# Kernel optimization log

Hardware: AMD Instinct MI355X
Metric: run time of the kernel (lower is better)

## Reference

```python
import jax, jax.numpy as jnp
import numpy as np

N, E = 25000, 400000
IN, HID, OUT = 128, 256, 128
T = 4                      # towers
F1, F2 = HID // T, OUT // T  # per-tower out dims (divide_input=False)
A = 12                     # len(aggregators)=4 * len(scalers)=3
EPS_STD = 1e-5
EPS_BN = 1e-5


def _glorot(k, shape):
    fin, fout = shape[-2], shape[-1]
    lim = float(np.sqrt(6.0 / (fin + fout)))
    return jax.random.uniform(k, shape, jnp.float32, -lim, lim)


def setup_inputs():
    key = jax.random.key(0)
    ks = jax.random.split(key, 10)
    x = jax.random.normal(ks[0], (N, IN), jnp.float32)
    edge_index = jax.random.randint(ks[1], (2, E), 0, N, dtype=jnp.int32)
    # avg_deg['log'] buffer of PNAConv: mean over nodes of log(deg+1)
    deg = jax.ops.segment_sum(jnp.ones((E,), jnp.float32), edge_index[1], num_segments=N)
    avg_log = jnp.mean(jnp.log(deg + 1.0)).astype(jnp.float32)
    return dict(
        x=x, edge_index=edge_index, avg_log=avg_log,
        pre1_W=_glorot(ks[2], (T, 2 * IN, F1)), pre1_b=jnp.zeros((T, F1), jnp.float32),
        post1_W=_glorot(ks[3], (T, IN + A * F1, F1)), post1_b=jnp.zeros((T, F1), jnp.float32),
        lin1_W=_glorot(ks[4], (T * F1, HID)), lin1_b=jnp.zeros((HID,), jnp.float32),
        bn1_g=jnp.ones((HID,), jnp.float32), bn1_b=jnp.zeros((HID,), jnp.float32),
        pre2_W=_glorot(ks[5], (T, 2 * HID, F2)), pre2_b=jnp.zeros((T, F2), jnp.float32),
        post2_W=_glorot(ks[6], (T, HID + A * F2, F2)), post2_b=jnp.zeros((T, F2), jnp.float32),
        lin2_W=_glorot(ks[7], (T * F2, OUT)), lin2_b=jnp.zeros((OUT,), jnp.float32),
        bn2_g=jnp.ones((OUT,), jnp.float32), bn2_b=jnp.zeros((OUT,), jnp.float32),
    )


def _pna(x, src, tgt, preW, preB, postW, postB, linW, linB, avg_log):
    """PNAConv: towers=T, divide_input=False, pre_layers=post_layers=1,
    aggregators [mean,min,max,std], scalers [identity,amplification,attenuation]."""
    n = x.shape[0]
    # message: per tower Linear on concat([x_i, x_j]) where i=target, j=source
    h = jnp.concatenate([x[tgt], x[src]], axis=-1)            # [E, 2*F_in]
    msg = jnp.einsum('ec,tcf->etf', h, preW) + preB           # [E, T, F]
    ones = jnp.ones((msg.shape[0],), msg.dtype)
    deg = jax.ops.segment_sum(ones, tgt, num_segments=n)      # in-degree [n]
    degc = jnp.maximum(deg, 1.0)[:, None, None]
    s1 = jax.ops.segment_sum(msg, tgt, num_segments=n)
    mean = s1 / degc
    s2 = jax.ops.segment_sum(msg * msg, tgt, num_segments=n)
    var = jnp.maximum(s2 / degc - mean * mean, 0.0)
    std = jnp.sqrt(var + EPS_STD)
    has = (deg > 0.0)[:, None, None]
    mn = jnp.where(has, jax.ops.segment_min(msg, tgt, num_segments=n), 0.0)
    mx = jnp.where(has, jax.ops.segment_max(msg, tgt, num_segments=n), 0.0)
    agg = jnp.concatenate([mean, mn, mx, std], axis=-1)       # [n, T, 4F]
    dlog = jnp.log(jnp.maximum(deg, 1.0) + 1.0)[:, None, None]
    out = jnp.concatenate([agg, agg * (dlog / avg_log), agg * (avg_log / dlog)], axis=-1)  # [n, T, 12F]
    xt = jnp.broadcast_to(x[:, None, :], (n, T, x.shape[-1]))
    post_in = jnp.concatenate([xt, out], axis=-1)             # [n, T, F_in + 12F]
    post = jnp.einsum('ntc,tcf->ntf', post_in, postW) + postB # [n, T, F]
    return post.reshape(n, -1) @ linW + linB                  # [n, out]


def _bn(x, g, b):
    # BatchNorm1d training-mode math: biased batch variance
    m = jnp.mean(x, axis=0)
    v = jnp.mean((x - m) ** 2, axis=0)
    return g * (x - m) / jnp.sqrt(v + EPS_BN) + b


def reference(x, edge_index, avg_log, pre1_W, pre1_b, post1_W, post1_b, lin1_W, lin1_b,
              bn1_g, bn1_b, pre2_W, pre2_b, post2_W, post2_b, lin2_W, lin2_b, bn2_g, bn2_b):
    src, tgt = edge_index[0], edge_index[1]
    h = _pna(x, src, tgt, pre1_W, pre1_b, post1_W, post1_b, lin1_W, lin1_b, avg_log)
    h = jax.nn.relu(_bn(jnp.nan_to_num(h), bn1_g, bn1_b))
    h = _pna(h, src, tgt, pre2_W, pre2_b, post2_W, post2_b, lin2_W, lin2_b, avg_log)
    h = jax.nn.relu(_bn(jnp.nan_to_num(h), bn2_g, bn2_b))
    return h
```

## Files before the change

### kernel.cpp

```cpp
#include <hip/hip_runtime.h>
#include <hip/hip_bf16.h>
#include <float.h>
#include <math.h>

typedef __hip_bfloat16 bf16;
typedef __attribute__((ext_vector_type(8))) short short8;
typedef __attribute__((ext_vector_type(4))) float f32x4;

__device__ __forceinline__ float bf2f(bf16 v){ return __bfloat162float(v); }
__device__ __forceinline__ void stv(float* p, float v){ *p = v; }
__device__ __forceinline__ void stv(bf16* p, float v){ *p = __float2bfloat16(v); }
__device__ __forceinline__ float nanfix(float v){
  if (v != v) return 0.f;
  return fminf(fmaxf(v, -FLT_MAX), FLT_MAX);
}
__device__ __forceinline__ unsigned short f2bu(float f){
  unsigned u = __float_as_uint(f);
  unsigned r = u + 0x7FFFu + ((u>>16)&1u);
  return (unsigned short)(r>>16);
}
template<int VEC>
__device__ __forceinline__ void ldbf(const bf16* p, float (&o)[VEC]){
  if constexpr (VEC==4){
    ushort4 r = *(const ushort4*)p;
    o[0]=__uint_as_float((unsigned)r.x<<16); o[1]=__uint_as_float((unsigned)r.y<<16);
    o[2]=__uint_as_float((unsigned)r.z<<16); o[3]=__uint_as_float((unsigned)r.w<<16);
  } else {
    ushort2 r = *(const ushort2*)p;
    o[0]=__uint_as_float((unsigned)r.x<<16); o[1]=__uint_as_float((unsigned)r.y<<16);
  }
}

__global__ void k_scan1(const int* __restrict__ deg, int* __restrict__ bsum, int N){
  __shared__ int sm[256];
  int i = blockIdx.x*256 + threadIdx.x;
  sm[threadIdx.x] = (i < N) ? deg[i] : 0;
  __syncthreads();
  for (int off = 128; off > 0; off >>= 1){
    if (threadIdx.x < off) sm[threadIdx.x] += sm[threadIdx.x + off];
    __syncthreads();
  }
  if (threadIdx.x == 0) bsum[blockIdx.x] = sm[0];
}

__global__ void k_scan2(int* __restrict__ bsum, int NB){
  __shared__ int sm[1024];
  int tid = threadIdx.x;
  sm[tid] = (tid < NB) ? bsum[tid] : 0;
  __syncthreads();
  for (int off = 1; off < 1024; off <<= 1){
    int t = (tid >= off) ? sm[tid-off] : 0;
    __syncthreads();
    sm[tid] += t;
    __syncthreads();
  }
  if (tid < NB) bsum[tid] = (tid == 0) ? 0 : sm[tid-1];
}

__global__ void k_scan3(const int* __restrict__ deg, const int* __restrict__ bsum,
                        int* __restrict__ offs, int N){
  __shared__ int sm[256];
  int tid = threadIdx.x;
  int i = blockIdx.x*256 + tid;
  int v = (i < N) ? deg[i] : 0;
  sm[tid] = v; __syncthreads();
  for (int off = 1; off < 256; off <<= 1){
    int t = (tid >= off) ? sm[tid-off] : 0;
    __syncthreads();
    sm[tid] += t;
    __syncthreads();
  }
  if (i < N) offs[i+1] = bsum[blockIdx.x] + sm[tid];
  if (i == 0) offs[0] = 0;
}

__global__ void k_scatter(const int* __restrict__ src, const int* __restrict__ tgt,
                          const int* __restrict__ offs, int* __restrict__ cnt,
                          int* __restrict__ ssrc, int E){
  int e = blockIdx.x*blockDim.x + threadIdx.x;
  if (e < E){
    int t = tgt[e];
    int pos = offs[t] + atomicAdd(&cnt[t], 1);
    ssrc[pos] = src[e];
  }
}

__device__ __forceinline__ void rp_pqT(const float* preW, const float* preB,
                                       bf16* WpqT, float* bpq, int K, int F, int idx){
  int NC = 4*F;
  int total = 2*NC*K;
  if (idx < total){
    int j = idx/K, c = idx%K;
    int half = j/NC, jj = j%NC, t = jj/F, f = jj%F;
    WpqT[idx] = __float2bfloat16(preW[(t*2*K + half*K + c)*F + f]);
  }
  if (idx < 2*NC) bpq[idx] = (idx < NC) ? preB[idx] : 0.f;
}
__device__ __forceinline__ void rp_xT(const float* postW, const float* postB,
                                      bf16* WxT, float* bpost, int KX, int F, int idx){
  int NC = 4*F; int KP = KX + 12*F;
  if (idx < NC*KX){
    int j = idx/KX, c = idx%KX, t = j/F, f = j%F;
    WxT[idx] = __float2bfloat16(postW[(t*KP + c)*F + f]);
  }
  if (idx < NC) bpost[idx] = postB[idx];
}
__device__ __forceinline__ void rp_agg3(const float* postW, bf16* Wagg3,
                                        int KX, int F, int idx){
  int K4F = 4*F; int KP = KX + 12*F;
  int total = 4*3*F*K4F;
  if (idx < total){
    int k = idx % K4F; int r = idx / K4F;
    int zr = r % (3*F); int t = r / (3*F);
    int s = zr / F, f = zr % F;
    Wagg3[idx] = __float2bfloat16(postW[((size_t)(t*KP + KX + s*K4F + k))*F + f]);
  }
}
__device__ __forceinline__ void rp_linT(const float* linW, bf16* WlinT,
                                        int K, int NC, int idx){
  if (idx < NC*K){
    int j = idx/K, c = idx%K;
    WlinT[idx] = __float2bfloat16(linW[c*NC + j]);
  }
}

struct SetupArgs {
  const float *pre1W, *pre1b, *post1W, *post1b, *lin1W;
  const float *pre2W, *pre2b, *post2W, *post2b, *lin2W;
  const float *x;
  const int *tgt;
  bf16 *WpqT1, *WxT1, *Wagg31, *lin1WT;
  bf16 *WpqT2, *WxT2, *Wagg32, *lin2WT;
  bf16 *x_bf;
  int *deg;
  float *bpq1, *bpost1, *bpq2, *bpost2;
  int nx4;
  int E;
  int gstride;
};

__global__ void k_setup(SetupArgs a){
  int idx = blockIdx.x*256 + threadIdx.x;
  switch (blockIdx.y){
    case 0: rp_pqT (a.pre1W, a.pre1b, a.WpqT1, a.bpq1, 128, 64, idx); break;
    case 1: rp_xT  (a.post1W, a.post1b, a.WxT1, a.bpost1, 128, 64, idx); break;
    case 2: rp_agg3(a.post1W, a.Wagg31, 128, 64, idx); break;
    case 3: rp_linT(a.lin1W, a.lin1WT, 256, 256, idx); break;
    case 4: rp_pqT (a.pre2W, a.pre2b, a.WpqT2, a.bpq2, 256, 32, idx); break;
    case 5: rp_xT  (a.post2W, a.post2b, a.WxT2, a.bpost2, 256, 32, idx); break;
    case 6: rp_agg3(a.post2W, a.Wagg32, 256, 32, idx); break;
    case 7: rp_linT(a.lin2W, a.lin2WT, 128, 128, idx); break;
    case 8:
      for (int i = idx; i < a.nx4; i += a.gstride){
        float4 v = *(const float4*)(a.x + (size_t)i*4);
        ushort4 o = make_ushort4(f2bu(v.x), f2bu(v.y), f2bu(v.z), f2bu(v.w));
        *(ushort4*)(a.x_bf + (size_t)i*4) = o;
      }
      break;
    case 9:
      for (int e = idx; e < a.E; e += a.gstride)
        atomicAdd(&a.deg[a.tgt[e]], 1);
      break;
  }
}

template<typename TO, bool STATS>
__global__ __launch_bounds__(256) void k_mgemm(
    const bf16* __restrict__ A, int lda,
    const bf16* __restrict__ Bt,
    const float* __restrict__ bias,
    TO* __restrict__ Cout, int ldc,
    int N, int K, int NC, float* __restrict__ part)
{
  __shared__ __align__(16) bf16 As[64*40];
  __shared__ __align__(16) bf16 Bs[64*40];
  __shared__ float sstat[4][2][16][2];
  int n0 = blockIdx.y*64;
  int j0 = blockIdx.x*64;
  int tid = threadIdx.x;
  int srow = tid>>2, skoff = (tid&3)*8;
  int wave = tid>>6, lane = tid&63;
  int wy = (wave>>1)*32, wx = (wave&1)*32;
  int l15 = lane&15, q = lane>>4;
  f32x4 acc[2][2] = {};
  for (int k0 = 0; k0 < K; k0 += 32){
    uint4 av = {0,0,0,0};
    int ar = n0 + srow;
    if (ar < N) av = *(const uint4*)(A + (size_t)ar*lda + k0 + skoff);
    *(uint4*)&As[srow*40 + skoff] = av;
    uint4 bv = {0,0,0,0};
    int br = j0 + srow;
    if (br < NC) bv = *(const uint4*)(Bt + (size_t)br*K + k0 + skoff);
    *(uint4*)&Bs[srow*40 + skoff] = bv;
    __syncthreads();
    short8 af[2], bfr[2];
    #pragma unroll
    for (int i = 0; i < 2; i++){
      af[i]  = *(const short8*)&As[(wy + i*16 + l15)*40 + q*8];
      bfr[i] = *(const short8*)&Bs[(wx + i*16 + l15)*40 + q*8];
    }
    #pragma unroll
    for (int mi = 0; mi < 2; mi++)
      #pragma unroll
      for (int ni = 0; ni < 2; ni++)
        acc[mi][ni] = __builtin_amdgcn_mfma_f32_16x16x32_bf16(af[mi], bfr[ni], acc[mi][ni], 0, 0, 0);
    __syncthreads();
  }
  float cs[2] = {0.f, 0.f}, cq[2] = {0.f, 0.f};
  #pragma unroll
  for (int mi = 0; mi < 2; mi++){
    #pragma unroll
    for (int ni = 0; ni < 2; ni++){
      #pragma unroll
      for (int r = 0; r < 4; r++){
        int n  = n0 + wy + mi*16 + q*4 + r;
        int jj = j0 + wx + ni*16 + l15;
        if (n < N && jj < NC){
          float v = acc[mi][ni][r] + bias[jj];
          stv(&Cout[(size_t)n*ldc + jj], v);
          if constexpr (STATS){ cs[ni] += v; cq[ni] = fmaf(v, v, cq[ni]); }
        }
      }
    }
  }
  if constexpr (STATS){
    #pragma unroll
    for (int ni = 0; ni < 2; ni++){
      float s = cs[ni], qq = cq[ni];
      s  += __shfl_xor(s, 16);  s  += __shfl_xor(s, 32);
      qq += __shfl_xor(qq, 16); qq += __shfl_xor(qq, 32);
      if (q == 0){ sstat[wave][ni][l15][0] = s; sstat[wave][ni][l15][1] = qq; }
    }
    __syncthreads();
    if (tid < 64){
      int j = tid;
      int wa = (j < 32) ? 0 : 1, wb = wa + 2;
      int ni = (j & 31) >> 4, li = j & 15;
      float s  = sstat[wa][ni][li][0] + sstat[wb][ni][li][0];
      float qq = sstat[wa][ni][li][1] + sstat[wb][ni][li][1];
      part[(size_t)blockIdx.y*2*ldc + (j0 + j)]       = s;
      part[(size_t)blockIdx.y*2*ldc + ldc + (j0 + j)] = qq;
    }
  }
}

template<int COLS>
__global__ __launch_bounds__(256) void k_postagg(
    const bf16* __restrict__ agg,
    const bf16* __restrict__ Wagg3,
    const bf16* __restrict__ PQX, int ldq, int cinOff,
    const float* __restrict__ scal,
    bf16* __restrict__ Cout, int ldc, int N)
{
  constexpr int K4F = 4*COLS;
  constexpr int ROWS3 = 3*COLS;
  constexpr int NI = COLS/32;
  constexpr int LDA_AGG = 16*COLS;
  __shared__ __align__(16) bf16 As[64*40];
  __shared__ __align__(16) bf16 Bs[ROWS3*40];
  int z = blockIdx.z;
  int n0 = blockIdx.y*64;
  int tid = threadIdx.x;
  int srow = tid>>2, skoff = (tid&3)*8;
  int wave = tid>>6, lane = tid&63;
  int wy = (wave>>1)*32;
  int wx = (wave&1)*(COLS/2);
  int l15 = lane&15, q = lane>>4;
  f32x4 acc[2][NI][3] = {};
  const bf16* Az = agg + (size_t)z*K4F;
  const bf16* Bz = Wagg3 + (size_t)z*ROWS3*K4F;
  for (int k0 = 0; k0 < K4F; k0 += 32){
    uint4 av = {0,0,0,0};
    int ar = n0 + srow;
    if (ar < N) av = *(const uint4*)(Az + (size_t)ar*LDA_AGG + k0 + skoff);
    *(uint4*)&As[srow*40 + skoff] = av;
    for (int r = srow; r < ROWS3; r += 64){
      uint4 bv = *(const uint4*)(Bz + (size_t)r*K4F + k0 + skoff);
      *(uint4*)&Bs[r*40 + skoff] = bv;
    }
    __syncthreads();
    short8 af[2];
    #pragma unroll
    for (int i = 0; i < 2; i++)
      af[i] = *(const short8*)&As[(wy + i*16 + l15)*40 + q*8];
    #pragma unroll
    for (int s = 0; s < 3; s++){
      #pragma unroll
      for (int ni = 0; ni < NI; ni++){
        short8 bfr = *(const short8*)&Bs[(s*COLS + wx + ni*16 + l15)*40 + q*8];
        #pragma unroll
        for (int mi = 0; mi < 2; mi++)
          acc[mi][ni][s] = __builtin_amdgcn_mfma_f32_16x16x32_bf16(af[mi], bfr, acc[mi][ni][s], 0, 0, 0);
      }
    }
    __syncthreads();
  }
  #pragma unroll
  for (int mi = 0; mi < 2; mi++){
    #pragma unroll
    for (int ni = 0; ni < NI; ni++){
      int jj = wx + ni*16 + l15;
      int jg = z*COLS + jj;
      #pragma unroll
      for (int r = 0; r < 4; r++){
        int n = n0 + wy + mi*16 + q*4 + r;
        if (n < N){
          float s1 = scal[2*n], s2 = scal[2*n+1];
          float cin = bf2f(PQX[(size_t)n*ldq + cinOff + jg]);
          float v = cin + acc[mi][ni][0][r] + s1*acc[mi][ni][1][r] + s2*acc[mi][ni][2][r];
          Cout[(size_t)n*ldc + jg] = __float2bfloat16(v);
        }
      }
    }
  }
}

template<int NC, int F>
__global__ __launch_bounds__(256) void k_agg(const bf16* __restrict__ PQ, int lda,
    const int* __restrict__ ssrc, const int* __restrict__ offs,
    const float* __restrict__ avgp,
    bf16* __restrict__ agg, float* __restrict__ scal, int N){
  constexpr int VEC = NC/64;
  int wave = threadIdx.x>>6, lane = threadIdx.x&63;
  int n = blockIdx.x*4 + wave;
  if (n >= N) return;
  int c0 = lane*VEC;
  float p[VEC];
  ldbf<VEC>(PQ + (size_t)n*lda + c0, p);
  int s0 = offs[n], s1 = offs[n+1];
  float sum[VEC], sq[VEC], mn[VEC], mx[VEC];
  #pragma unroll
  for (int v=0;v<VEC;v++){ sum[v]=0.f; sq[v]=0.f; mn[v]=FLT_MAX; mx[v]=-FLT_MAX; }
  const bf16* Q = PQ + NC + c0;
  int i = s0;
  for (; i+7 < s1; i += 8){
    int se[8];
    #pragma unroll
    for (int u=0;u<8;u++) se[u] = ssrc[i+u];
    float qv[8][VEC];
    #pragma unroll
    for (int u=0;u<8;u++) ldbf<VEC>(Q + (size_t)se[u]*lda, qv[u]);
    #pragma unroll
    for (int u=0;u<8;u++){
      #pragma unroll
      for (int v=0;v<VEC;v++){
        float qq = qv[u][v];
        sum[v] += qq; sq[v] = fmaf(qq,qq,sq[v]);
        mn[v] = fminf(mn[v], qq); mx[v] = fmaxf(mx[v], qq);
      }
    }
  }
  for (; i+3 < s1; i += 4){
    int se[4];
    #pragma unroll
    for (int u=0;u<4;u++) se[u] = ssrc[i+u];
    float qv[4][VEC];
    #pragma unroll
    for (int u=0;u<4;u++) ldbf<VEC>(Q + (size_t)se[u]*lda, qv[u]);
    #pragma unroll
    for (int u=0;u<4;u++){
      #pragma unroll
      for (int v=0;v<VEC;v++){
        float qq = qv[u][v];
        sum[v] += qq; sq[v] = fmaf(qq,qq,sq[v]);
        mn[v] = fminf(mn[v], qq); mx[v] = fmaxf(mx[v], qq);
      }
    }
  }
  for (; i < s1; i++){
    int sa = ssrc[i];
    float qa[VEC];
    ldbf<VEC>(Q + (size_t)sa*lda, qa);
    #pragma unroll
    for (int v=0;v<VEC;v++){
      float qq = qa[v];
      sum[v]+=qq; sq[v]=fmaf(qq,qq,sq[v]); mn[v]=fminf(mn[v],qq); mx[v]=fmaxf(mx[v],qq);
    }
  }
  int deg = s1-s0;
  float degf = (float)deg;
  float degc = fmaxf(degf, 1.f);
  unsigned short um[VEC], un[VEC], ux[VEC], us[VEC];
  #pragma unroll
  for (int v=0;v<VEC;v++){
    float pv = p[v];
    float sum_m = fmaf(degf, pv, sum[v]);
    float sq_m  = sq[v] + 2.f*pv*sum[v] + degf*pv*pv;
    float mean = sum_m/degc;
    float var = fmaxf(sq_m/degc - mean*mean, 0.f);
    float sd = sqrtf(var + 1e-5f);
    float mnv = deg>0 ? pv + mn[v] : 0.f;
    float mxv = deg>0 ? pv + mx[v] : 0.f;
    um[v]=f2bu(mean); un[v]=f2bu(mnv); ux[v]=f2bu(mxv); us[v]=f2bu(sd);
  }
  int t = c0 / F, f0 = c0 % F;
  bf16* base = agg + (size_t)n*4*NC + (size_t)t*4*F + f0;
  if constexpr (VEC==4){
    *(ushort4*)(base)       = make_ushort4(um[0],um[1],um[2],um[3]);
    *(ushort4*)(base + F)   = make_ushort4(un[0],un[1],un[2],un[3]);
    *(ushort4*)(base + 2*F) = make_ushort4(ux[0],ux[1],ux[2],ux[3]);
    *(ushort4*)(base + 3*F) = make_ushort4(us[0],us[1],us[2],us[3]);
  } else {
    *(ushort2*)(base)       = make_ushort2(um[0],um[1]);
    *(ushort2*)(base + F)   = make_ushort2(un[0],un[1]);
    *(ushort2*)(base + 2*F) = make_ushort2(ux[0],ux[1]);
    *(ushort2*)(base + 3*F) = make_ushort2(us[0],us[1]);
  }
  if (lane==0){
    float dlog = logf(degc + 1.f);
    float avg = *avgp;
    scal[2*n]   = dlog/avg;
    scal[2*n+1] = avg/dlog;
  }
}

template<int C>
__global__ __launch_bounds__(256) void k_bn_final(const float* __restrict__ part, int PB,
                                                  float* __restrict__ stats){
  int c = blockIdx.x*256 + threadIdx.x;
  if (c >= 2*C) return;
  int CH = gridDim.y;
  int per = (PB + CH - 1)/CH;
  int p0 = blockIdx.y*per, p1 = min(p0 + per, PB);
  float acc = 0.f;
  int p = p0;
  for (; p+4 <= p1; p += 4){
    acc += part[(size_t)p*2*C + c] + part[(size_t)(p+1)*2*C + c]
         + part[(size_t)(p+2)*2*C + c] + part[(size_t)(p+3)*2*C + c];
  }
  for (; p < p1; p++) acc += part[(size_t)p*2*C + c];
  atomicAdd(&stats[c], acc);
}

template<typename TO, int C>
__global__ void k_bn_apply(const bf16* __restrict__ h, const float* __restrict__ stats,
     const float* __restrict__ g, const float* __restrict__ b,
     TO* __restrict__ out, int N){
  int idx = blockIdx.x*blockDim.x + threadIdx.x;
  if (idx >= N*(C/4)) return;
  int c = (idx % (C/4))*4;
  float fn = (float)N;
  float v[4];
  ldbf<4>(h + (size_t)idx*4, v);
  float r[4];
  #pragma unroll
  for (int k = 0; k < 4; k++){
    float m = stats[c+k]/fn;
    float var = fmaxf(stats[C+c+k]/fn - m*m, 0.f);
    float inv = rsqrtf(var + 1e-5f);
    float vv = nanfix(v[k]);
    r[k] = fmaxf(g[c+k]*(vv - m)*inv + b[c+k], 0.f);
  }
  if constexpr (sizeof(TO) == 4){
    float4 o = {r[0], r[1], r[2], r[3]};
    *(float4*)((float*)out + (size_t)idx*4) = o;
  } else {
    ushort4 o = make_ushort4(f2bu(r[0]), f2bu(r[1]), f2bu(r[2]), f2bu(r[3]));
    *(ushort4*)((bf16*)out + (size_t)idx*4) = o;
  }
}

static inline int cdiv(int a, int b){ return (a + b - 1)/b; }

extern "C" void kernel_launch(void* const* d_in, const int* in_sizes, int n_in,
                              void* d_out, int out_size, void* d_ws, size_t ws_size,
                              hipStream_t stream){
  const int IN = 128, HID = 256, T = 4, F1 = 64, F2 = 32;
  const int N = in_sizes[0]/IN;
  const int E = in_sizes[1]/2;
  const int NC1 = T*F1;
  const int NC2 = T*F2;
  const int LDQ1 = 2*NC1 + NC1;
  const int LDQ2 = 2*NC2 + NC2;

  const float* x      = (const float*)d_in[0];
  const int*   ei     = (const int*)  d_in[1];
  const int*   srcE   = ei;
  const int*   tgtE   = ei + E;
  const float* avgp   = (const float*)d_in[2];
  const float* pre1W  = (const float*)d_in[3];
  const float* pre1b  = (const float*)d_in[4];
  const float* post1W = (const float*)d_in[5];
  const float* post1b = (const float*)d_in[6];
  const float* lin1W  = (const float*)d_in[7];
  const float* lin1b  = (const float*)d_in[8];
  const float* bn1g   = (const float*)d_in[9];
  const float* bn1b   = (const float*)d_in[10];
  const float* pre2W  = (const float*)d_in[11];
  const float* pre2b  = (const float*)d_in[12];
  const float* post2W = (const float*)d_in[13];
  const float* post2b = (const float*)d_in[14];
  const float* lin2W  = (const float*)d_in[15];
  const float* lin2b  = (const float*)d_in[16];
  const float* bn2g   = (const float*)d_in[17];
  const float* bn2b   = (const float*)d_in[18];

  char* w = (char*)d_ws;
  auto alloc = [&](size_t bytes)->void*{
    void* p = (void*)w; w += (bytes + 255) & ~(size_t)255; return p;
  };
  bf16* BT1    = (bf16*)alloc((size_t)LDQ1*IN*2);
  bf16* WpqT1  = BT1;              bf16* WxT1 = BT1 + (size_t)2*NC1*IN;
  float* bias1 = (float*)alloc((size_t)LDQ1*4);
  float* bpq1  = bias1;            float* bpost1 = bias1 + 2*NC1;
  bf16* Wagg31 = (bf16*)alloc((size_t)T*3*F1*4*F1*2);
  bf16* lin1WT = (bf16*)alloc((size_t)HID*NC1*2);
  bf16* BT2    = (bf16*)alloc((size_t)LDQ2*HID*2);
  bf16* WpqT2  = BT2;              bf16* WxT2 = BT2 + (size_t)2*NC2*HID;
  float* bias2 = (float*)alloc((size_t)LDQ2*4);
  float* bpq2  = bias2;            float* bpost2 = bias2 + 2*NC2;
  bf16* Wagg32 = (bf16*)alloc((size_t)T*3*F2*4*F2*2);
  bf16* lin2WT = (bf16*)alloc((size_t)128*NC2*2);
  int* deg_i   = (int*)alloc((size_t)N*4);
  int* cnt     = (int*)alloc((size_t)N*4);
  float* stats = (float*)alloc(1024*4);
  size_t zbytes = (size_t)((char*)stats - (char*)deg_i) + 1024*4;
  int* offs    = (int*)alloc((size_t)(N+1)*4);
  int* bsum    = (int*)alloc((size_t)cdiv(N,256)*4);
  int* ssrc    = (int*)alloc((size_t)E*4);
  bf16* x_bf   = (bf16*)alloc((size_t)N*IN*2);
  bf16* PQX    = (bf16*)alloc((size_t)N*LDQ1*2);
  bf16* aggb   = (bf16*)alloc((size_t)N*4*NC1*2);
  float* scal  = (float*)alloc((size_t)N*2*4);
  bf16* postbb = (bf16*)alloc((size_t)N*256*2);
  bf16* hpre   = (bf16*)alloc((size_t)N*256*2);
  bf16* h1b    = (bf16*)alloc((size_t)N*256*2);
  int NB = cdiv(N,64);
  float* part  = (float*)alloc((size_t)NB*512*4);

  hipMemsetAsync(deg_i, 0, zbytes, stream);

  int sgx = cdiv(T*3*F1*4*F1, 256);
  SetupArgs sa = { pre1W, pre1b, post1W, post1b, lin1W,
                   pre2W, pre2b, post2W, post2b, lin2W,
                   x, tgtE,
                   WpqT1, WxT1, Wagg31, lin1WT,
                   WpqT2, WxT2, Wagg32, lin2WT,
                   x_bf, deg_i,
                   bpq1, bpost1, bpq2, bpost2,
                   N*IN/4, E, sgx*256 };
  k_setup<<<dim3(sgx, 10),256,0,stream>>>(sa);

  int NBs = cdiv(N,256);
  k_scan1<<<NBs,256,0,stream>>>(deg_i, bsum, N);
  k_scan2<<<1,1024,0,stream>>>(bsum, NBs);
  k_scan3<<<NBs,256,0,stream>>>(deg_i, bsum, offs, N);
  k_scatter<<<cdiv(E,256),256,0,stream>>>(srcE, tgtE, offs, cnt, ssrc, E);

  k_mgemm<bf16,false><<<dim3(LDQ1/64,NB),256,0,stream>>>(x_bf, IN, BT1, bias1, PQX, LDQ1, N, IN, LDQ1, nullptr);
  k_agg<256,64><<<cdiv(N,4),256,0,stream>>>(PQX, LDQ1, ssrc, offs, avgp, aggb, scal, N);
  k_postagg<64><<<dim3(1,NB,T),256,0,stream>>>(aggb, Wagg31, PQX, LDQ1, 2*NC1, scal,
                                               postbb, NC1, N);
  k_mgemm<bf16,true><<<dim3(4,NB),256,0,stream>>>(postbb, NC1, lin1WT, lin1b, hpre, HID, N, NC1, HID, part);
  k_bn_final<256><<<dim3(2,4),256,0,stream>>>(part, NB, stats);
  k_bn_apply<bf16,256><<<cdiv(N*64,256),256,0,stream>>>(hpre, stats, bn1g, bn1b, h1b, N);

  k_mgemm<bf16,false><<<dim3(LDQ2/64,NB),256,0,stream>>>(h1b, HID, BT2, bias2, PQX, LDQ2, N, HID, LDQ2, nullptr);
  k_agg<128,32><<<cdiv(N,4),256,0,stream>>>(PQX, LDQ2, ssrc, offs, avgp, aggb, scal, N);
  k_postagg<32><<<dim3(1,NB,T),256,0,stream>>>(aggb, Wagg32, PQX, LDQ2, 2*NC2, scal,
                                               postbb, NC2, N);
  k_mgemm<bf16,true><<<dim3(2,NB),256,0,stream>>>(postbb, NC2, lin2WT, lin2b, hpre, 128, N, NC2, 128, part);
  k_bn_final<128><<<dim3(1,4),256,0,stream>>>(part, NB, stats + 512);
  k_bn_apply<float,128><<<cdiv(N*32,256),256,0,stream>>>(hpre, stats + 512, bn2g, bn2b, (float*)d_out, N);
}
```

Baseline: 371.6 us.

## Double-buffer GEMM tiles with direct global-to-LDS async loads

Both the message/linear GEMM kernel and the post-aggregation GEMM kernel now load A and B tiles with global_load_lds straight into LDS instead of going through registers. The tiles are double-buffered so the next k-step's load is issued while the current step's MFMAs run, hiding global-memory latency. In exchange, the LDS row padding is removed (stride 32 instead of 40), which can add bank conflicts on fragment reads. The row-bounds checks on A and B are also gone, so the last partial row tile now reads past N unless the buffers are padded.

```diff
diff --git a/kernel.cpp b/kernel.cpp
--- a/kernel.cpp
+++ b/kernel.cpp
@@ -29,6 +29,12 @@
     ushort2 r = *(const ushort2*)p;
     o[0]=__uint_as_float((unsigned)r.x<<16); o[1]=__uint_as_float((unsigned)r.y<<16);
   }
+}
+
+__device__ __forceinline__ void gl_lds16(const bf16* g, bf16* l){
+  __builtin_amdgcn_global_load_lds(
+      (const __attribute__((address_space(1))) void*)g,
+      (__attribute__((address_space(3))) void*)l, 16, 0, 0);
 }
 
 __global__ void k_scan1(const int* __restrict__ deg, int* __restrict__ bsum, int N){
@@ -172,8 +178,8 @@
     TO* __restrict__ Cout, int ldc,
     int N, int K, int NC, float* __restrict__ part)
 {
-  __shared__ __align__(16) bf16 As[64*40];
-  __shared__ __align__(16) bf16 Bs[64*40];
+  __shared__ __align__(16) bf16 As[2][64*32];
+  __shared__ __align__(16) bf16 Bs[2][64*32];
   __shared__ float sstat[4][2][16][2];
   int n0 = blockIdx.y*64;
   int j0 = blockIdx.x*64;
@@ -183,21 +189,23 @@
   int wy = (wave>>1)*32, wx = (wave&1)*32;
   int l15 = lane&15, q = lane>>4;
   f32x4 acc[2][2] = {};
-  for (int k0 = 0; k0 < K; k0 += 32){
-    uint4 av = {0,0,0,0};
-    int ar = n0 + srow;
-    if (ar < N) av = *(const uint4*)(A + (size_t)ar*lda + k0 + skoff);
-    *(uint4*)&As[srow*40 + skoff] = av;
-    uint4 bv = {0,0,0,0};
-    int br = j0 + srow;
-    if (br < NC) bv = *(const uint4*)(Bt + (size_t)br*K + k0 + skoff);
-    *(uint4*)&Bs[srow*40 + skoff] = bv;
-    __syncthreads();
+  const bf16* Ag = A  + (size_t)(n0 + srow)*lda + skoff;
+  const bf16* Bg = Bt + (size_t)(j0 + srow)*K   + skoff;
+  int nt = K >> 5;
+  gl_lds16(Ag, &As[0][tid*8]);
+  gl_lds16(Bg, &Bs[0][tid*8]);
+  __syncthreads();
+  for (int t = 0; t < nt; t++){
+    int cur = t & 1;
+    if (t + 1 < nt){
+      gl_lds16(Ag + (t+1)*32, &As[cur^1][tid*8]);
+      gl_lds16(Bg + (t+1)*32, &Bs[cur^1][tid*8]);
+    }
     short8 af[2], bfr[2];
     #pragma unroll
     for (int i = 0; i < 2; i++){
-      af[i]  = *(const short8*)&As[(wy + i*16 + l15)*40 + q*8];
-      bfr[i] = *(const short8*)&Bs[(wx + i*16 + l15)*40 + q*8];
+      af[i]  = *(const short8*)&As[cur][(wy + i*16 + l15)*32 + q*8];
+      bfr[i] = *(const short8*)&Bs[cur][(wx + i*16 + l15)*32 + q*8];
     }
     #pragma unroll
     for (int mi = 0; mi < 2; mi++)
@@ -256,8 +264,8 @@
   constexpr int ROWS3 = 3*COLS;
   constexpr int NI = COLS/32;
   constexpr int LDA_AGG = 16*COLS;
-  __shared__ __align__(16) bf16 As[64*40];
-  __shared__ __align__(16) bf16 Bs[ROWS3*40];
+  __shared__ __align__(16) bf16 As[2][64*32];
+  __shared__ __align__(16) bf16 Bs[2][ROWS3*32];
   int z = blockIdx.z;
   int n0 = blockIdx.y*64;
   int tid = threadIdx.x;
@@ -267,27 +275,35 @@
   int wx = (wave&1)*(COLS/2);
   int l15 = lane&15, q = lane>>4;
   f32x4 acc[2][NI][3] = {};
-  const bf16* Az = agg + (size_t)z*K4F;
-  const bf16* Bz = Wagg3 + (size_t)z*ROWS3*K4F;
-  for (int k0 = 0; k0 < K4F; k0 += 32){
-    uint4 av = {0,0,0,0};
-    int ar = n0 + srow;
-    if (ar < N) av = *(const uint4*)(Az + (size_t)ar*LDA_AGG + k0 + skoff);
-    *(uint4*)&As[srow*40 + skoff] = av;
-    for (int r = srow; r < ROWS3; r += 64){
-      uint4 bv = *(const uint4*)(Bz + (size_t)r*K4F + k0 + skoff);
-      *(uint4*)&Bs[r*40 + skoff] = bv;
-    }
-    __syncthreads();
+  const bf16* Ag = agg + (size_t)z*K4F + (size_t)(n0 + srow)*LDA_AGG + skoff;
+  const bf16* Bg = Wagg3 + (size_t)z*ROWS3*K4F + (size_t)srow*K4F + skoff;
+  constexpr int NT = K4F/32;
+  gl_lds16(Ag, &As[0][tid*8]);
+  #pragma unroll
+  for (int r = 0; r < ROWS3/64 + ((ROWS3%64)?1:0); r++){
+    int rr = srow + r*64;
+    if (rr < ROWS3) gl_lds16(Bg + (size_t)r*64*K4F, &Bs[0][rr*32 + skoff]);
+  }
+  __syncthreads();
+  for (int t = 0; t < NT; t++){
+    int cur = t & 1;
+    if (t + 1 < NT){
+      gl_lds16(Ag + (t+1)*32, &As[cur^1][tid*8]);
+      #pragma unroll
+      for (int r = 0; r < ROWS3/64 + ((ROWS3%64)?1:0); r++){
+        int rr = srow + r*64;
+        if (rr < ROWS3) gl_lds16(Bg + (size_t)r*64*K4F + (t+1)*32, &Bs[cur^1][rr*32 + skoff]);
+      }
+    }
     short8 af[2];
     #pragma unroll
     for (int i = 0; i < 2; i++)
-      af[i] = *(const short8*)&As[(wy + i*16 + l15)*40 + q*8];
+      af[i] = *(const short8*)&As[cur][(wy + i*16 + l15)*32 + q*8];
     #pragma unroll
     for (int s = 0; s < 3; s++){
       #pragma unroll
       for (int ni = 0; ni < NI; ni++){
-        short8 bfr = *(const short8*)&Bs[(s*COLS + wx + ni*16 + l15)*40 + q*8];
+        short8 bfr = *(const short8*)&Bs[cur][(s*COLS + wx + ni*16 + l15)*32 + q*8];
         #pragma unroll
         for (int mi = 0; mi < 2; mi++)
           acc[mi][ni][s] = __builtin_amdgcn_mfma_f32_16x16x32_bf16(af[mi], bfr, acc[mi][ni][s], 0, 0, 0);
```

Result: faster. 359.4 us (-3.3%).
